# Performance work log

Measured on AMD Instinct MI355X. Metric: run time of the kernel, lower is better.

## Reference

```python
import jax, jax.numpy as jnp
import numpy as np

DIM = 1024
HEADS = 16
HEAD_DIM = DIM // HEADS
NEG = -1e30
EPS = 1e-5


def _linear(x, w, b):
    # torch nn.Linear: y = x @ W^T + b, W: [out, in]
    return jnp.einsum('bnd,od->bno', x, w) + b


def _mha(x, ctx, wq, bq, wk, bk, wv, bv, wo, bo, mask):
    B, N, D = x.shape
    M = ctx.shape[1]
    q = _linear(x, wq, bq).reshape(B, N, HEADS, HEAD_DIM).transpose(0, 2, 1, 3)
    k = _linear(ctx, wk, bk).reshape(B, M, HEADS, HEAD_DIM).transpose(0, 2, 1, 3)
    v = _linear(ctx, wv, bv).reshape(B, M, HEADS, HEAD_DIM).transpose(0, 2, 1, 3)
    scores = jnp.einsum('bhqd,bhkd->bhqk', q, k) / np.sqrt(HEAD_DIM).astype(np.float32)
    if mask is not None:
        scores = jnp.where(mask == 0, NEG, scores)
    attn = jax.nn.softmax(scores, axis=-1)  # dropout = identity (eval mode)
    out = jnp.einsum('bhqk,bhkd->bhqd', attn, v)
    out = out.transpose(0, 2, 1, 3).reshape(B, N, D)
    return _linear(out, wo, bo)


def _ln(x, g, b):
    mu = jnp.mean(x, axis=-1, keepdims=True)
    var = jnp.mean(jnp.square(x - mu), axis=-1, keepdims=True)
    return (x - mu) * jax.lax.rsqrt(var + EPS) * g + b


def setup_inputs() -> dict:
    key = jax.random.key(0)
    ks = jax.random.split(key, 24)
    B, N, M = 2, 2048, 1024
    s = 0.02
    d = {
        'x': jax.random.normal(ks[0], (B, N, DIM), jnp.float32),
        'memory': jax.random.normal(ks[1], (B, M, DIM), jnp.float32),
        'mask': jnp.tril(jnp.ones((N, N), jnp.int32))[None, None],
    }
    i = 2
    for p in ['sa', 'ca']:
        for nm in ['q', 'k', 'v', 'o']:
            d[f'{p}_w{nm}'] = jax.random.normal(ks[i], (DIM, DIM), jnp.float32) * s; i += 1
            d[f'{p}_b{nm}'] = jnp.zeros((DIM,), jnp.float32)
    d['ff_w1'] = jax.random.normal(ks[i], (4 * DIM, DIM), jnp.float32) * s; i += 1
    d['ff_b1'] = jnp.zeros((4 * DIM,), jnp.float32)
    d['ff_w2'] = jax.random.normal(ks[i], (DIM, 4 * DIM), jnp.float32) * s; i += 1
    d['ff_b2'] = jnp.zeros((DIM,), jnp.float32)
    for j in (1, 2, 3):
        d[f'ln{j}_g'] = jnp.ones((DIM,), jnp.float32)
        d[f'ln{j}_b'] = jnp.zeros((DIM,), jnp.float32)
    return d


def reference(x, memory, mask,
              sa_wq, sa_bq, sa_wk, sa_bk, sa_wv, sa_bv, sa_wo, sa_bo,
              ca_wq, ca_bq, ca_wk, ca_bk, ca_wv, ca_bv, ca_wo, ca_bo,
              ff_w1, ff_b1, ff_w2, ff_b2,
              ln1_g, ln1_b, ln2_g, ln2_b, ln3_g, ln3_b):
    x = _ln(x + _mha(x, x, sa_wq, sa_bq, sa_wk, sa_bk, sa_wv, sa_bv, sa_wo, sa_bo, mask), ln1_g, ln1_b)
    x = _ln(x + _mha(x, memory, ca_wq, ca_bq, ca_wk, ca_bk, ca_wv, ca_bv, ca_wo, ca_bo, None), ln2_g, ln2_b)
    h = jax.nn.relu(_linear(x, ff_w1, ff_b1))  # dropout = identity (eval)
    x = _ln(x + _linear(h, ff_w2, ff_b2), ln3_g, ln3_b)
    return x
```

## Files before the change

kernel.cpp:

```cpp
#include <hip/hip_runtime.h>


typedef __attribute__((ext_vector_type(8))) short bf16x8;
typedef __attribute__((ext_vector_type(4))) float f32x4;

__device__ __forceinline__ unsigned short f2bf(float f) {
    union { float f; unsigned int u; } v; v.f = f;
    unsigned int r = v.u + 0x7fffu + ((v.u >> 16) & 1u);
    return (unsigned short)(r >> 16);
}
__device__ __forceinline__ float bf2f(unsigned short u) {
    union { unsigned int u; float f; } v; v.u = (unsigned int)u << 16;
    return v.f;
}
__device__ __forceinline__ unsigned int bftrunc(float f) {
    union { float f; unsigned int u; } v; v.f = f;
    return v.u >> 16;
}

struct ConvArgs {
    const float* src[12];
    unsigned short* dst[12];
    int blk_ofs[13];
    int n4[12];
    const float* bq; const float* bk; const float* bv;
    const float* ck; const float* cv;
    float* bqkv; float* bkvc;
};
__global__ __launch_bounds__(256) void conv_multi(ConvArgs a)
{
    int bid = blockIdx.x;
    if (bid >= a.blk_ofs[12]) {
        int i = (bid - a.blk_ofs[12]) * 256 + threadIdx.x;
        if (i < 1024)       a.bqkv[i] = a.bq[i];
        else if (i < 2048)  a.bqkv[i] = a.bk[i - 1024];
        else if (i < 3072)  a.bqkv[i] = a.bv[i - 2048];
        else if (i < 4096)  a.bkvc[i - 3072] = a.ck[i - 3072];
        else if (i < 5120)  a.bkvc[i - 3072] = a.cv[i - 4096];
        return;
    }
    int s = 0;
#pragma unroll
    for (int t = 0; t < 12; ++t) if (bid >= a.blk_ofs[t + 1]) s = t + 1;
    int i = (bid - a.blk_ofs[s]) * 256 + threadIdx.x;
    if (i >= a.n4[s]) return;
    float4 v = ((const float4*)a.src[s])[i];
    ushort4 o;
    o.x = f2bf(v.x); o.y = f2bf(v.y); o.z = f2bf(v.z); o.w = f2bf(v.w);
    ((ushort4*)a.dst[s])[i] = o;
}

template<int TM, int TN, int EPI, int SK>
__device__ __forceinline__ void gemm_body(
    unsigned short (*As)[64], unsigned short (*Bs)[64],
    const unsigned short* __restrict__ A, const unsigned short* __restrict__ W,
    const float* __restrict__ bias, unsigned short* __restrict__ out,
    int K, int Ncols, long slice_stride, int bid, int gx, int zslice)
{
    constexpr int AI = TM / 32;
    constexpr int BJ = TN / 32;

    const int tid  = threadIdx.x;
    const int lane = tid & 63;
    const int wave = tid >> 6;
    const int qd   = lane >> 4;
    const int l15  = lane & 15;
    const int wm   = (wave >> 1) * (TM / 2);
    const int wn   = (wave & 1) * (TN / 2);

    const int gpg = 8 * gx;
    const long m0 = (long)((bid / gpg) * 8 + (bid & 7)) * TM;
    const long n0 = (long)((bid % gpg) >> 3) * TN;

    f32x4 acc[AI][BJ] = {};

    const int srow = lane >> 3;
    const int scol = (((lane & 7) ^ srow)) * 8;
    const unsigned short* Ag = A + (m0 + wave * (8 * AI) + srow) * (long)K + scol;
    const unsigned short* Wg = W + (n0 + wave * (8 * BJ) + srow) * (long)K + scol;

    const int ksl   = K / SK;
    const int kbase = (SK > 1) ? zslice * ksl : 0;

    for (int k0 = kbase; k0 < kbase + ksl; k0 += 64) {
#pragma unroll
        for (int c = 0; c < AI; ++c)
            __builtin_amdgcn_global_load_lds(
                (const __attribute__((address_space(1))) unsigned int*)(Ag + (long)c * 8 * K + k0),
                (__attribute__((address_space(3))) unsigned int*)((char*)&As[0][0] + (wave * AI + c) * 1024),
                16, 0, 0);
#pragma unroll
        for (int c = 0; c < BJ; ++c)
            __builtin_amdgcn_global_load_lds(
                (const __attribute__((address_space(1))) unsigned int*)(Wg + (long)c * 8 * K + k0),
                (__attribute__((address_space(3))) unsigned int*)((char*)&Bs[0][0] + (wave * BJ + c) * 1024),
                16, 0, 0);
        __syncthreads();
#pragma unroll
        for (int kk = 0; kk < 64; kk += 32) {
            const int pg = ((((kk >> 3) + qd)) ^ (l15 & 7)) * 8;
            bf16x8 af[AI], bw[BJ];
#pragma unroll
            for (int i = 0; i < AI; ++i)
                af[i] = *(const bf16x8*)&As[wm + i * 16 + l15][pg];
#pragma unroll
            for (int j = 0; j < BJ; ++j)
                bw[j] = *(const bf16x8*)&Bs[wn + j * 16 + l15][pg];
#pragma unroll
            for (int i = 0; i < AI; ++i)
#pragma unroll
                for (int j = 0; j < BJ; ++j)
                    acc[i][j] = __builtin_amdgcn_mfma_f32_16x16x32_bf16(
                        af[i], bw[j], acc[i][j], 0, 0, 0);
        }
        __syncthreads();
    }

    unsigned short* op = out + ((SK > 1) ? (long)zslice * slice_stride : 0);
#pragma unroll
    for (int j = 0; j < BJ; ++j) {
        long col = n0 + wn + j * 16 + l15;
        float bv = (SK == 1 || zslice == 0) ? bias[col] : 0.f;
#pragma unroll
        for (int i = 0; i < AI; ++i) {
#pragma unroll
            for (int r = 0; r < 4; ++r) {
                long row = m0 + wm + i * 16 + qd * 4 + r;
                float v = acc[i][j][r] + bv;
                if (EPI == 1) v = (v > 0.f) ? v : 0.f;
                op[row * Ncols + col] = f2bf(v);
            }
        }
    }
}

template<int TM, int TN, int EPI, int SK>
__global__ __launch_bounds__(256) void gemm_bt(
    const unsigned short* __restrict__ A, const unsigned short* __restrict__ W,
    const float* __restrict__ bias, unsigned short* __restrict__ out,
    int K, int Ncols, long slice_stride)
{
    __shared__ unsigned short As[TM][64];
    __shared__ unsigned short Bs[TN][64];
    const int bid = blockIdx.y * gridDim.x + blockIdx.x;
    gemm_body<TM, TN, EPI, SK>(As, Bs, A, W, bias, out, K, Ncols, slice_stride,
                               bid, gridDim.x, (int)blockIdx.z);
}

template<int TM, int TN>
__global__ __launch_bounds__(256) void gemm_bt_dual(
    const unsigned short* A0, const unsigned short* W0, const float* b0,
    unsigned short* o0, int K0, int N0, int gx0, int nb0,
    const unsigned short* A1, const unsigned short* W1, const float* b1,
    unsigned short* o1, int K1, int N1, int gx1)
{
    __shared__ unsigned short As[TM][64];
    __shared__ unsigned short Bs[TN][64];
    const int bid = blockIdx.x;
    if (bid < nb0)
        gemm_body<TM, TN, 0, 1>(As, Bs, A0, W0, b0, o0, K0, N0, 0, bid, gx0, 0);
    else
        gemm_body<TM, TN, 0, 1>(As, Bs, A1, W1, b1, o1, K1, N1, 0, bid - nb0, gx1, 0);
}

__global__ __launch_bounds__(256) void attn_kernel(
    const unsigned short* __restrict__ Qb, int q_stride,
    const unsigned short* __restrict__ KVb, int kv_stride, int koff, int voff,
    unsigned short* __restrict__ O,
    int Nq, int Mk, int causal)
{
    __shared__ unsigned short Ks[64][72];
    __shared__ unsigned short Vs[64][72];
    __shared__ unsigned short Ps[4][16][72];

    const int tid  = threadIdx.x;
    const int lane = tid & 63;
    const int wave = tid >> 6;
    const int qd   = lane >> 4;
    const int l15  = lane & 15;
    const int h    = blockIdx.y;
    const int b    = blockIdx.z;
    int jq = blockIdx.x;
    if (causal && (b & 1)) jq = gridDim.x - 1 - jq;
    const int q0 = jq * 64;
    const int tb = q0 + wave * 16;

    bf16x8 aq0, aq1;
    {
        const unsigned short* qp =
            Qb + (long)(b * Nq + tb + l15) * q_stride + h * 64 + qd * 8;
        aq0 = *(const bf16x8*)qp;
        aq1 = *(const bf16x8*)(qp + 32);
    }

    float lpart[4] = {};
    f32x4 oacc[4] = {};

    const int krow = tid >> 3;
    const int kcol = (tid & 7) * 8;
    const int vj   = tid & 31;
    const int va_k = (vj & 15) + ((vj & 16) << 1);
    const int vfg  = (tid >> 5) * 8;
    const int vpc  = (va_k & 15) * 4 + (va_k >> 4);

    const unsigned short* Kg = KVb + (long)b * Mk * kv_stride + koff + h * 64;
    const unsigned short* Vg = KVb + (long)b * Mk * kv_stride + voff + h * 64;

    bf16x8 kr0, kr1, vra, vrb;
    auto prefetch = [&](int k0) {
        kr0 = *(const bf16x8*)(Kg + (long)(k0 + krow) * kv_stride + kcol);
        kr1 = *(const bf16x8*)(Kg + (long)(k0 + krow + 32) * kv_stride + kcol);
        const unsigned short* v0 = Vg + (long)(k0 + va_k) * kv_stride + vfg;
        vra = *(const bf16x8*)v0;
        vrb = *(const bf16x8*)(v0 + 16 * kv_stride);
    };

    const int nk = causal ? (q0 + 64) : Mk;
    prefetch(0);
    const float SCL = 0.125f * 1.44269504f;

    for (int k0 = 0; k0 < nk; k0 += 64) {
        __syncthreads();
        *(bf16x8*)&Ks[krow][kcol]      = kr0;
        *(bf16x8*)&Ks[krow + 32][kcol] = kr1;
#pragma unroll
        for (int jf = 0; jf < 8; ++jf) {
            unsigned int d = (unsigned short)vra[jf] |
                             ((unsigned int)(unsigned short)vrb[jf] << 16);
            *(unsigned int*)&Vs[vfg + jf][vpc] = d;
        }
        if (k0 + 64 < nk) prefetch(k0 + 64);
        __syncthreads();

        if (!causal || (k0 <= tb + 15)) {
            bf16x8 bk[4][2];
#pragma unroll
            for (int kt = 0; kt < 4; ++kt)
#pragma unroll
                for (int c = 0; c < 2; ++c)
                    bk[kt][c] = *(const bf16x8*)&Ks[kt * 16 + l15][c * 32 + qd * 8];
            f32x4 s[4];
#pragma unroll
            for (int kt = 0; kt < 4; ++kt) {
                f32x4 z = {};
                z = __builtin_amdgcn_mfma_f32_16x16x32_bf16(aq0, bk[kt][0], z, 0, 0, 0);
                z = __builtin_amdgcn_mfma_f32_16x16x32_bf16(aq1, bk[kt][1], z, 0, 0, 0);
                s[kt] = z;
            }
            const bool needmask = causal && (k0 + 63 > tb);
#pragma unroll
            for (int r = 0; r < 4; ++r) {
                const int qg = tb + qd * 4 + r;
                float e[4];
#pragma unroll
                for (int kt = 0; kt < 4; ++kt) {
                    float ev = __builtin_amdgcn_exp2f(s[kt][r] * SCL);
                    if (needmask && (k0 + kt * 16 + l15 > qg)) ev = 0.f;
                    e[kt] = ev;
                }
                lpart[r] += (e[0] + e[1]) + (e[2] + e[3]);
                unsigned int lo = bftrunc(e[0]) | (bftrunc(e[1]) << 16);
                unsigned int hi = bftrunc(e[2]) | (bftrunc(e[3]) << 16);
                uint2 pk; pk.x = lo; pk.y = hi;
                *(uint2*)&Ps[wave][qd * 4 + r][l15 * 4] = pk;
            }
            bf16x8 bv[4][2];
#pragma unroll
            for (int dt = 0; dt < 4; ++dt)
#pragma unroll
                for (int c = 0; c < 2; ++c)
                    bv[dt][c] = *(const bf16x8*)&Vs[dt * 16 + l15][c * 32 + qd * 8];
            bf16x8 ap0 = *(const bf16x8*)&Ps[wave][l15][qd * 8];
            bf16x8 ap1 = *(const bf16x8*)&Ps[wave][l15][32 + qd * 8];
#pragma unroll
            for (int dt = 0; dt < 4; ++dt) {
                oacc[dt] = __builtin_amdgcn_mfma_f32_16x16x32_bf16(
                    ap0, bv[dt][0], oacc[dt], 0, 0, 0);
                oacc[dt] = __builtin_amdgcn_mfma_f32_16x16x32_bf16(
                    ap1, bv[dt][1], oacc[dt], 0, 0, 0);
            }
        }
    }

#pragma unroll
    for (int r = 0; r < 4; ++r) {
        float l = lpart[r];
        l += __shfl_xor(l, 1);
        l += __shfl_xor(l, 2);
        l += __shfl_xor(l, 4);
        l += __shfl_xor(l, 8);
        float inv = 1.f / l;
        long row = (long)(b * Nq + tb + qd * 4 + r);
#pragma unroll
        for (int dt = 0; dt < 4; ++dt)
            O[row * 1024 + h * 64 + dt * 16 + l15] = f2bf(oacc[dt][r] * inv);
    }
}

template<int ND, int RESBF>
__global__ __launch_bounds__(256) void ln_res_kernel(
    const void* __restrict__ res, const unsigned short* __restrict__ delta,
    long dstride, const float* __restrict__ g, const float* __restrict__ beta,
    float* __restrict__ yout, unsigned short* __restrict__ ybf)
{
    __shared__ float red[8];
    const int row = blockIdx.x;
    const int tid = threadIdx.x;
    const long base = (long)row * 1024 + tid * 4;
    float v0, v1, v2, v3;
    if (RESBF) {
        ushort4 a = *(const ushort4*)((const unsigned short*)res + base);
        v0 = bf2f(a.x); v1 = bf2f(a.y); v2 = bf2f(a.z); v3 = bf2f(a.w);
    } else {
        float4 a = *(const float4*)((const float*)res + base);
        v0 = a.x; v1 = a.y; v2 = a.z; v3 = a.w;
    }
#pragma unroll
    for (int t = 0; t < ND; ++t) {
        ushort4 d = *(const ushort4*)(delta + t * dstride + base);
        v0 += bf2f(d.x); v1 += bf2f(d.y); v2 += bf2f(d.z); v3 += bf2f(d.w);
    }
    float s  = v0 + v1 + v2 + v3;
    float ss = v0 * v0 + v1 * v1 + v2 * v2 + v3 * v3;
#pragma unroll
    for (int off = 1; off < 64; off <<= 1) {
        s  += __shfl_xor(s, off);
        ss += __shfl_xor(ss, off);
    }
    const int wave = tid >> 6;
    if ((tid & 63) == 0) { red[wave] = s; red[4 + wave] = ss; }
    __syncthreads();
    float st  = red[0] + red[1] + red[2] + red[3];
    float sst = red[4] + red[5] + red[6] + red[7];
    float mean = st * (1.f / 1024.f);
    float var  = sst * (1.f / 1024.f) - mean * mean;
    float inv  = rsqrtf(var + 1e-5f);
    const int c = tid * 4;
    float y0 = (v0 - mean) * inv * g[c + 0] + beta[c + 0];
    float y1 = (v1 - mean) * inv * g[c + 1] + beta[c + 1];
    float y2 = (v2 - mean) * inv * g[c + 2] + beta[c + 2];
    float y3 = (v3 - mean) * inv * g[c + 3] + beta[c + 3];
    if (yout) *(float4*)(yout + base) = make_float4(y0, y1, y2, y3);
    if (ybf) {
        ushort4 o;
        o.x = f2bf(y0); o.y = f2bf(y1); o.z = f2bf(y2); o.w = f2bf(y3);
        *(ushort4*)(ybf + base) = o;
    }
}

extern "C" void kernel_launch(void* const* d_in, const int* in_sizes, int n_in,
                              void* d_out, int out_size, void* d_ws, size_t ws_size,
                              hipStream_t stream)
{
    const int B = 2, N = 2048, M = 1024, D = 1024, FF = 4096;
    const int TN = B * N;
    const int TM = B * M;
    const size_t MB = 1024 * 1024;

    const float* x     = (const float*)d_in[0];
    const float* mem   = (const float*)d_in[1];
    const float* sa_wq = (const float*)d_in[3];  const float* sa_bq = (const float*)d_in[4];
    const float* sa_wk = (const float*)d_in[5];  const float* sa_bk = (const float*)d_in[6];
    const float* sa_wv = (const float*)d_in[7];  const float* sa_bv = (const float*)d_in[8];
    const float* sa_wo = (const float*)d_in[9];  const float* sa_bo = (const float*)d_in[10];
    const float* ca_wq = (const float*)d_in[11]; const float* ca_bq = (const float*)d_in[12];
    const float* ca_wk = (const float*)d_in[13]; const float* ca_bk = (const float*)d_in[14];
    const float* ca_wv = (const float*)d_in[15]; const float* ca_bv = (const float*)d_in[16];
    const float* ca_wo = (const float*)d_in[17]; const float* ca_bo = (const float*)d_in[18];
    const float* ff_w1 = (const float*)d_in[19]; const float* ff_b1 = (const float*)d_in[20];
    const float* ff_w2 = (const float*)d_in[21]; const float* ff_b2 = (const float*)d_in[22];
    const float* ln1_g = (const float*)d_in[23]; const float* ln1_b = (const float*)d_in[24];
    const float* ln2_g = (const float*)d_in[25]; const float* ln2_b = (const float*)d_in[26];
    const float* ln3_g = (const float*)d_in[27]; const float* ln3_b = (const float*)d_in[28];

    char* w = (char*)d_ws;
    size_t off = 0;
    auto alloc = [&](size_t bytes) -> char* {
        char* p = w + off; off += (bytes + 255) & ~(size_t)255; return p;
    };

    unsigned short* xb   = (unsigned short*)alloc((size_t)TN * D * 2);
    unsigned short* memb = (unsigned short*)alloc((size_t)TM * D * 2);
    unsigned short* wqkv = (unsigned short*)alloc((size_t)3 * D * D * 2);
    unsigned short* wos  = (unsigned short*)alloc((size_t)D * D * 2);
    unsigned short* wqc  = (unsigned short*)alloc((size_t)D * D * 2);
    unsigned short* wkvc = (unsigned short*)alloc((size_t)2 * D * D * 2);
    unsigned short* woc  = (unsigned short*)alloc((size_t)D * D * 2);
    unsigned short* w1b  = (unsigned short*)alloc((size_t)FF * D * 2);
    unsigned short* w2b  = (unsigned short*)alloc((size_t)D * FF * 2);
    char* big = alloc((size_t)80 * MB);
    unsigned short* qkv   = (unsigned short*)big;
    unsigned short* ab    = (unsigned short*)(big + 24 * MB);
    unsigned short* kvb   = (unsigned short*)(big + 32 * MB);
    unsigned short* qb    = (unsigned short*)(big + 40 * MB);
    unsigned short* hb    = (unsigned short*)big;
    unsigned short* tmpbf = (unsigned short*)(big + 48 * MB);
    const long      TSL   = (long)TN * D;
    float* bqkv = (float*)alloc((size_t)3 * D * 4);
    float* bkvc = (float*)alloc((size_t)2 * D * 4);

    ConvArgs ca;
    const float* srcs[12] = {x, mem, sa_wq, sa_wk, sa_wv, sa_wo,
                             ca_wq, ca_wk, ca_wv, ca_wo, ff_w1, ff_w2};
    unsigned short* dsts[12] = {xb, memb, wqkv, wqkv + (size_t)D * D,
                                wqkv + (size_t)2 * D * D, wos, wqc, wkvc,
                                wkvc + (size_t)D * D, woc, w1b, w2b};
    long ns[12] = {(long)TN * D, (long)TM * D, (long)D * D, (long)D * D,
                   (long)D * D, (long)D * D, (long)D * D, (long)D * D,
                   (long)D * D, (long)D * D, (long)FF * D, (long)D * FF};
    int total_blk = 0;
    for (int i = 0; i < 12; ++i) {
        ca.src[i] = srcs[i]; ca.dst[i] = dsts[i];
        ca.n4[i] = (int)(ns[i] / 4);
        ca.blk_ofs[i] = total_blk;
        total_blk += (ca.n4[i] + 255) / 256;
    }
    ca.blk_ofs[12] = total_blk;
    ca.bq = sa_bq; ca.bk = sa_bk; ca.bv = sa_bv; ca.ck = ca_bk; ca.cv = ca_bv;
    ca.bqkv = bqkv; ca.bkvc = bkvc;
    conv_multi<<<dim3(total_blk + 20), dim3(256), 0, stream>>>(ca);

    dim3 blk(256);

    gemm_bt_dual<128, 64><<<dim3(2048), blk, 0, stream>>>(
        xb,   wqkv, bqkv, qkv, D, 3 * D, 3 * D / 64, 1536,
        memb, wkvc, bkvc, kvb, D, 2 * D, 2 * D / 64);

    attn_kernel<<<dim3(N / 64, 16, B), blk, 0, stream>>>(
        qkv, 3 * D, qkv, 3 * D, D, 2 * D, ab, N, N, 1);
    gemm_bt<128, 64, 0, 2><<<dim3(D / 64, TN / 128, 2), blk, 0, stream>>>(
        ab, wos, sa_bo, tmpbf, D, D, TSL);
    ln_res_kernel<2, 0><<<dim3(TN), blk, 0, stream>>>(
        x, tmpbf, TSL, ln1_g, ln1_b, nullptr, xb);

    gemm_bt<128, 64, 0, 1><<<dim3(D / 64, TN / 128), blk, 0, stream>>>(
        xb, wqc, ca_bq, qb, D, D, 0);
    attn_kernel<<<dim3(N / 64, 16, B), blk, 0, stream>>>(
        qb, D, kvb, 2 * D, 0, D, ab, N, M, 0);
    gemm_bt<128, 64, 0, 2><<<dim3(D / 64, TN / 128, 2), blk, 0, stream>>>(
        ab, woc, ca_bo, tmpbf, D, D, TSL);
    ln_res_kernel<2, 1><<<dim3(TN), blk, 0, stream>>>(
        xb, tmpbf, TSL, ln2_g, ln2_b, nullptr, xb);

    gemm_bt<128, 64, 1, 1><<<dim3(FF / 64, TN / 128), blk, 0, stream>>>(
        xb, w1b, ff_b1, hb, D, FF, 0);
    gemm_bt<128, 64, 0, 4><<<dim3(D / 64, TN / 128, 4), blk, 0, stream>>>(
        hb, w2b, ff_b2, tmpbf, FF, D, TSL);
    ln_res_kernel<4, 1><<<dim3(TN), blk, 0, stream>>>(
        xb, tmpbf, TSL, ln3_g, ln3_b, (float*)d_out, nullptr);
}
```

Measured before the change: 482.5 us.

## Add 256x256-tile 8-wave GEMM with direct-to-LDS double-buffered loads

Introduces a new GEMM body using 256x256 output tiles computed by 512 threads (8 waves). Operand tiles go straight from global memory into XOR-swizzled, double-buffered LDS via global_load_lds. The k-loop is split into four phases that interleave prefetch, barriers and MFMA bursts, with s_setprio raising priority around the MFMA bursts. The QKV/KV projection dual GEMM and both FFN GEMMs now use it, cutting block counts and increasing operand reuse. The cost is 128KB of dynamic LDS per block, roughly one block per CU, and more fragile hand-written wait counts.

```diff
diff --git a/kernel.cpp b/kernel.cpp
--- a/kernel.cpp
+++ b/kernel.cpp
@@ -147,20 +147,200 @@
                                bid, gridDim.x, (int)blockIdx.z);
 }
 
-template<int TM, int TN>
-__global__ __launch_bounds__(256) void gemm_bt_dual(
+template<int EPI, int SK>
+__device__ __forceinline__ void gemm8_body(
+    unsigned short* Ab, unsigned short* Bb,
+    const unsigned short* __restrict__ A, const unsigned short* __restrict__ W,
+    const float* __restrict__ bias, unsigned short* __restrict__ out,
+    int K, int Ncols, long slice_stride, int bid, int gx, int zslice)
+{
+    const int tid  = threadIdx.x;
+    const int lane = tid & 63;
+    const int wave = tid >> 6;
+    const int qd   = lane >> 4;
+    const int l15  = lane & 15;
+    const int wm   = (wave >> 2) * 128;
+    const int wn   = (wave & 3) * 64;
+
+    const int gpg = 8 * gx;
+    const long m0 = (long)((bid / gpg) * 8 + (bid & 7)) * 256;
+    const long n0 = (long)((bid % gpg) >> 3) * 256;
+
+    const int ksl   = K / SK;
+    const int kbase = (SK > 1) ? zslice * ksl : 0;
+    const int NG    = ksl / 64;
+
+    f32x4 acc[8][4] = {};
+
+    const int srow = tid >> 3;
+    const int sgrp = ((tid & 7) ^ (srow & 7)) * 8;
+    const unsigned short* Ag = A + (m0 + srow) * (long)K + kbase + sgrp;
+    const unsigned short* Wg = W + (n0 + srow) * (long)K + kbase + sgrp;
+
+    auto stA = [&](int db, int r0, int kt) {
+        __builtin_amdgcn_global_load_lds(
+            (const __attribute__((address_space(1))) unsigned int*)(Ag + (long)r0 * K + kt * 64),
+            (__attribute__((address_space(3))) unsigned int*)(Ab + db * 16384 + r0 * 64 + wave * 512),
+            16, 0, 0);
+    };
+    auto stB = [&](int db, int r0, int kt) {
+        __builtin_amdgcn_global_load_lds(
+            (const __attribute__((address_space(1))) unsigned int*)(Wg + (long)r0 * K + kt * 64),
+            (__attribute__((address_space(3))) unsigned int*)(Bb + db * 16384 + r0 * 64 + wave * 512),
+            16, 0, 0);
+    };
+    auto rdA = [&](int db, int row, int kk) -> bf16x8 {
+        const int p = (((kk << 2) + qd) ^ (l15 & 7)) << 3;
+        return *(const bf16x8*)(Ab + db * 16384 + row * 64 + p);
+    };
+    auto rdB = [&](int db, int row, int kk) -> bf16x8 {
+        const int p = (((kk << 2) + qd) ^ (l15 & 7)) << 3;
+        return *(const bf16x8*)(Bb + db * 16384 + row * 64 + p);
+    };
+
+#pragma unroll
+    for (int h = 0; h < 4; ++h) stA(0, h * 64, 0);
+#pragma unroll
+    for (int h = 0; h < 4; ++h) stB(0, h * 64, 0);
+    if (NG > 1) {
+#pragma unroll
+        for (int h = 0; h < 4; ++h) stA(1, h * 64, 1);
+#pragma unroll
+        for (int h = 0; h < 4; ++h) stB(1, h * 64, 1);
+        asm volatile("s_waitcnt vmcnt(8)" ::: "memory");
+    } else {
+        asm volatile("s_waitcnt vmcnt(0)" ::: "memory");
+    }
+    __builtin_amdgcn_s_barrier();
+
+    for (int g = 0; g < NG; ++g) {
+        const int db = g & 1, nb = db ^ 1;
+        const bool pf1 = (g >= 1) && (g + 1 < NG);
+        const bool pf2 = (g + 2 < NG);
+        bf16x8 af[4][2], bw[4][2];
+
+#pragma unroll
+        for (int i = 0; i < 4; ++i)
+#pragma unroll
+            for (int kk = 0; kk < 2; ++kk)
+                af[i][kk] = rdA(db, wm + i * 16 + l15, kk);
+#pragma unroll
+        for (int j = 0; j < 2; ++j)
+#pragma unroll
+            for (int kk = 0; kk < 2; ++kk)
+                bw[j][kk] = rdB(db, wn + j * 16 + l15, kk);
+        if (pf1) { stA(nb, 64, g + 1); stA(nb, 192, g + 1); }
+        __builtin_amdgcn_s_barrier();
+        asm volatile("s_waitcnt lgkmcnt(0)" ::: "memory");
+        __builtin_amdgcn_sched_barrier(0);
+        __builtin_amdgcn_s_setprio(1);
+#pragma unroll
+        for (int i = 0; i < 4; ++i)
+#pragma unroll
+            for (int j = 0; j < 2; ++j) {
+                acc[i][j] = __builtin_amdgcn_mfma_f32_16x16x32_bf16(af[i][0], bw[j][0], acc[i][j], 0, 0, 0);
+                acc[i][j] = __builtin_amdgcn_mfma_f32_16x16x32_bf16(af[i][1], bw[j][1], acc[i][j], 0, 0, 0);
+            }
+        __builtin_amdgcn_s_setprio(0);
+        __builtin_amdgcn_s_barrier();
+
+#pragma unroll
+        for (int j = 2; j < 4; ++j)
+#pragma unroll
+            for (int kk = 0; kk < 2; ++kk)
+                bw[j][kk] = rdB(db, wn + j * 16 + l15, kk);
+        if (pf1) { stB(nb, 0, g + 1); stB(nb, 64, g + 1); }
+        __builtin_amdgcn_s_barrier();
+        asm volatile("s_waitcnt lgkmcnt(0)" ::: "memory");
+        __builtin_amdgcn_sched_barrier(0);
+        __builtin_amdgcn_s_setprio(1);
+#pragma unroll
+        for (int i = 0; i < 4; ++i)
+#pragma unroll
+            for (int j = 2; j < 4; ++j) {
+                acc[i][j] = __builtin_amdgcn_mfma_f32_16x16x32_bf16(af[i][0], bw[j][0], acc[i][j], 0, 0, 0);
+                acc[i][j] = __builtin_amdgcn_mfma_f32_16x16x32_bf16(af[i][1], bw[j][1], acc[i][j], 0, 0, 0);
+            }
+        __builtin_amdgcn_s_setprio(0);
+        __builtin_amdgcn_s_barrier();
+
+#pragma unroll
+        for (int i = 0; i < 4; ++i)
+#pragma unroll
+            for (int kk = 0; kk < 2; ++kk)
+                af[i][kk] = rdA(db, wm + 64 + i * 16 + l15, kk);
+        if (pf1) { stB(nb, 128, g + 1); stB(nb, 192, g + 1); }
+        __builtin_amdgcn_s_barrier();
+        asm volatile("s_waitcnt lgkmcnt(0)" ::: "memory");
+        __builtin_amdgcn_sched_barrier(0);
+        __builtin_amdgcn_s_setprio(1);
+#pragma unroll
+        for (int i = 0; i < 4; ++i)
+#pragma unroll
+            for (int j = 0; j < 2; ++j) {
+                acc[4 + i][j] = __builtin_amdgcn_mfma_f32_16x16x32_bf16(af[i][0], bw[j][0], acc[4 + i][j], 0, 0, 0);
+                acc[4 + i][j] = __builtin_amdgcn_mfma_f32_16x16x32_bf16(af[i][1], bw[j][1], acc[4 + i][j], 0, 0, 0);
+            }
+        __builtin_amdgcn_s_setprio(0);
+        __builtin_amdgcn_s_barrier();
+
+        if (pf2) { stA(db, 0, g + 2); stA(db, 128, g + 2); }
+        __builtin_amdgcn_s_setprio(1);
+#pragma unroll
+        for (int i = 0; i < 4; ++i)
+#pragma unroll
+            for (int j = 2; j < 4; ++j) {
+                acc[4 + i][j] = __builtin_amdgcn_mfma_f32_16x16x32_bf16(af[i][0], bw[j][0], acc[4 + i][j], 0, 0, 0);
+                acc[4 + i][j] = __builtin_amdgcn_mfma_f32_16x16x32_bf16(af[i][1], bw[j][1], acc[4 + i][j], 0, 0, 0);
+            }
+        __builtin_amdgcn_s_setprio(0);
+        if (pf2)             { asm volatile("s_waitcnt vmcnt(2)" ::: "memory"); }
+        else if (g + 1 < NG) { asm volatile("s_waitcnt vmcnt(0)" ::: "memory"); }
+        __builtin_amdgcn_s_barrier();
+    }
+
+    unsigned short* op = out + ((SK > 1) ? (long)zslice * slice_stride : 0);
+#pragma unroll
+    for (int j = 0; j < 4; ++j) {
+        long col = n0 + wn + j * 16 + l15;
+        float bv = (SK == 1 || zslice == 0) ? bias[col] : 0.f;
+#pragma unroll
+        for (int i = 0; i < 8; ++i) {
+#pragma unroll
+            for (int r = 0; r < 4; ++r) {
+                long row = m0 + wm + (i >> 2) * 64 + (i & 3) * 16 + qd * 4 + r;
+                float v = acc[i][j][r] + bv;
+                if (EPI == 1) v = (v > 0.f) ? v : 0.f;
+                op[row * Ncols + col] = f2bf(v);
+            }
+        }
+    }
+}
+
+template<int EPI, int SK>
+__global__ __launch_bounds__(512) void gemm8_bt(
+    const unsigned short* __restrict__ A, const unsigned short* __restrict__ W,
+    const float* __restrict__ bias, unsigned short* __restrict__ out,
+    int K, int Ncols, long slice_stride)
+{
+    extern __shared__ unsigned short smem[];
+    const int bid = blockIdx.y * gridDim.x + blockIdx.x;
+    gemm8_body<EPI, SK>(smem, smem + 32768, A, W, bias, out, K, Ncols,
+                        slice_stride, bid, gridDim.x, (int)blockIdx.z);
+}
+
+__global__ __launch_bounds__(512) void gemm8_dual(
     const unsigned short* A0, const unsigned short* W0, const float* b0,
     unsigned short* o0, int K0, int N0, int gx0, int nb0,
     const unsigned short* A1, const unsigned short* W1, const float* b1,
     unsigned short* o1, int K1, int N1, int gx1)
 {
-    __shared__ unsigned short As[TM][64];
-    __shared__ unsigned short Bs[TN][64];
+    extern __shared__ unsigned short smem[];
     const int bid = blockIdx.x;
     if (bid < nb0)
-        gemm_body<TM, TN, 0, 1>(As, Bs, A0, W0, b0, o0, K0, N0, 0, bid, gx0, 0);
+        gemm8_body<0, 1>(smem, smem + 32768, A0, W0, b0, o0, K0, N0, 0, bid, gx0, 0);
     else
-        gemm_body<TM, TN, 0, 1>(As, Bs, A1, W1, b1, o1, K1, N1, 0, bid - nb0, gx1, 0);
+        gemm8_body<0, 1>(smem, smem + 32768, A1, W1, b1, o1, K1, N1, 0, bid - nb0, gx1, 0);
 }
 
 __global__ __launch_bounds__(256) void attn_kernel(
@@ -421,10 +601,12 @@
     conv_multi<<<dim3(total_blk + 20), dim3(256), 0, stream>>>(ca);
 
     dim3 blk(256);
-
-    gemm_bt_dual<128, 64><<<dim3(2048), blk, 0, stream>>>(
-        xb,   wqkv, bqkv, qkv, D, 3 * D, 3 * D / 64, 1536,
-        memb, wkvc, bkvc, kvb, D, 2 * D, 2 * D / 64);
+    dim3 blk8(512);
+    const unsigned int LDS8 = 131072;
+
+    gemm8_dual<<<dim3(256), blk8, LDS8, stream>>>(
+        xb,   wqkv, bqkv, qkv, D, 3 * D, 12, 192,
+        memb, wkvc, bkvc, kvb, D, 2 * D, 8);
 
     attn_kernel<<<dim3(N / 64, 16, B), blk, 0, stream>>>(
         qkv, 3 * D, qkv, 3 * D, D, 2 * D, ab, N, N, 1);
@@ -442,9 +624,9 @@
     ln_res_kernel<2, 1><<<dim3(TN), blk, 0, stream>>>(
         xb, tmpbf, TSL, ln2_g, ln2_b, nullptr, xb);
 
-    gemm_bt<128, 64, 1, 1><<<dim3(FF / 64, TN / 128), blk, 0, stream>>>(
+    gemm8_bt<1, 1><<<dim3(FF / 256, TN / 256), blk8, LDS8, stream>>>(
         xb, w1b, ff_b1, hb, D, FF, 0);
-    gemm_bt<128, 64, 0, 4><<<dim3(D / 64, TN / 128, 4), blk, 0, stream>>>(
+    gemm8_bt<0, 4><<<dim3(D / 256, TN / 256, 4), blk8, LDS8, stream>>>(
         hb, w2b, ff_b2, tmpbf, FF, D, TSL);
     ln_res_kernel<4, 1><<<dim3(TN), blk, 0, stream>>>(
         xb, tmpbf, TSL, ln3_g, ln3_b, (float*)d_out, nullptr);
```

New measurement: 481.0 us. Within noise of the previous version (-0.3%).
